# Performance work log

Measured on AMD Instinct MI355X. Metric: run time of the kernel, lower is better.

## Reference

```python
import jax, jax.numpy as jnp
import numpy as np

H = 1024
B_SZ = 4
L = 2048


def setup_inputs() -> dict:
    key = jax.random.key(0)
    ks = jax.random.split(key, 7)
    s_in = 1.0 / np.sqrt(H)
    x = jax.random.normal(ks[0], (B_SZ, L, H), dtype=jnp.float32)
    # torch nn.Linear weights: (out_features, in_features)
    W_proj = jax.random.uniform(ks[1], (4 * H, H), minval=-s_in, maxval=s_in, dtype=jnp.float32)
    W_delta = jax.random.uniform(ks[2], (H, H), minval=-s_in, maxval=s_in, dtype=jnp.float32)
    b_delta = jax.random.uniform(ks[3], (H,), minval=-s_in, maxval=s_in, dtype=jnp.float32)
    A = 0.02 * jax.random.normal(ks[4], (1, 1, H), dtype=jnp.float32)
    Bp = 0.02 * jax.random.normal(ks[5], (1, H, 1), dtype=jnp.float32)
    D = jnp.ones((1,), dtype=jnp.float32)
    return {"x": x, "W_proj": W_proj, "A": A, "Bp": Bp, "D": D, "W_delta": W_delta, "b_delta": b_delta}


def reference(x, W_proj, A, Bp, D, W_delta, b_delta):
    # x: (b, l, h)
    h = x.shape[-1]
    proj = x @ W_proj.T                                   # (b, l, 4h)
    delta, Bs, Cs, residual = jnp.split(proj, 4, axis=-1) # each (b, l, h)
    delta = jax.nn.softplus(delta @ W_delta.T + b_delta)  # (b, l, h)
    A1 = A[0, 0]       # (h,)
    B1 = Bp[0, :, 0]   # (h,)
    # discretization: dA[b,h,l] = exp(delta*A)[b,l,h] * B1[h] (n-dim of Bp has size 1)
    dA = jnp.exp(delta * A1) * B1                         # (b, l, h), layout transposed vs torch
    # dB[b,h,0,l] = cumsum_l(delta[b,l,h] * B1[h])
    dB = jnp.cumsum(delta * B1, axis=1)                   # (b, l, h)
    # selective_scan: y[b,h,l] = sum_n (dA[b,h,l]*u[b,h,n] + dB[b,h,0,l]) * C[b,h,n]
    # sum over n distributes: y = dA * sum_n(u*C) + dB * sum_n(C)
    uC = jnp.sum(x * Cs, axis=1, keepdims=True)           # (b, 1, h)
    Csum = jnp.sum(Cs, axis=1, keepdims=True)             # (b, 1, h)
    y = dA * uC + dB * Csum                               # (b, l, h)
    return y + residual * D
```

## Files before the change

### kernel.cpp

```cpp
#include <hip/hip_runtime.h>
#include <hip/hip_bf16.h>
#include <cstdint>

#define H 1024
#define BSZ 4
#define LSEQ 2048
#define M_TOT (BSZ*LSEQ)
#define NCH 32
#define LCH (LSEQ/NCH)

typedef __attribute__((ext_vector_type(4))) float  f32x4;
typedef __attribute__((ext_vector_type(2))) float  f32x2;
typedef __attribute__((ext_vector_type(8))) __bf16 bf16x8;
typedef __attribute__((ext_vector_type(4))) __bf16 bf16x4;
typedef __attribute__((ext_vector_type(2))) __bf16 bf16x2;

typedef __attribute__((address_space(1))) unsigned int as1_u32;
typedef __attribute__((address_space(3))) unsigned int as3_u32;

__device__ __forceinline__ void gld_lds16(const void* g, const void* l) {
    as1_u32* gp = reinterpret_cast<as1_u32*>((uintptr_t)g);
    as3_u32* lp = reinterpret_cast<as3_u32*>((uint32_t)(uintptr_t)l);
    __builtin_amdgcn_global_load_lds(gp, lp, 16, 0, 0);
}

template<int KT, int MODE>
__global__ __launch_bounds__(256, 3) void gemm_bt(
    const __bf16* __restrict__ A,
    const __bf16* __restrict__ B,
    __bf16* __restrict__ O0,
    __bf16* __restrict__ O2,
    const __bf16* __restrict__ xb,
    const float* __restrict__ bias,
    float* __restrict__ pD,
    float* __restrict__ pU,
    float* __restrict__ pC)
{
    constexpr int K = KT * 32;
    __shared__ __align__(16) __bf16 lds[17408];

    const int tid  = threadIdx.x;
    const int lane = tid & 63;
    const int wid  = tid >> 6;
    const int wr   = (wid >> 1) * 64;
    const int wc   = (wid & 1) * 64;
    const int l15  = lane & 15;
    const int quad = lane >> 4;

    const int row0 = blockIdx.y * 128;
    const int col0 = blockIdx.x * 128;

    const int srow = lane >> 2;
    const int soct = (lane & 3) ^ ((lane >> 3) & 3);
    const __bf16* ag0 = A + (size_t)(row0 + (wid    )*16 + srow) * K + soct*8;
    const __bf16* ag1 = A + (size_t)(row0 + (wid + 4)*16 + srow) * K + soct*8;
    const __bf16* bg0 = B + (size_t)(col0 + (wid    )*16 + srow) * K + soct*8;
    const __bf16* bg1 = B + (size_t)(col0 + (wid + 4)*16 + srow) * K + soct*8;
    const int lA0 = (wid    )*512;
    const int lA1 = (wid + 4)*512;
    const int lB0 = 4096 + (wid    )*512;
    const int lB1 = 4096 + (wid + 4)*512;

    const int sw = (l15 >> 1) & 3;
    int aoff[4], boff[4];
#pragma unroll
    for (int i = 0; i < 4; ++i) {
        aoff[i] =        ((wr + i*16 + l15) * 4 + (quad ^ sw)) * 8;
        boff[i] = 4096 + ((wc + i*16 + l15) * 4 + (quad ^ sw)) * 8;
    }

    f32x4 acc[4][4] = {};

    auto stage = [&](int buf) {
        __bf16* base = lds + buf * 8192;
        gld_lds16(ag0, base + lA0);
        gld_lds16(ag1, base + lA1);
        gld_lds16(bg0, base + lB0);
        gld_lds16(bg1, base + lB1);
        ag0 += 32; ag1 += 32; bg0 += 32; bg1 += 32;
    };
    auto compute = [&](int buf) {
        const __bf16* base = lds + buf * 8192;
        bf16x8 af[4], bf[4];
#pragma unroll
        for (int i = 0; i < 4; ++i) af[i] = *(const bf16x8*)(base + aoff[i]);
#pragma unroll
        for (int j = 0; j < 4; ++j) bf[j] = *(const bf16x8*)(base + boff[j]);
#pragma unroll
        for (int i = 0; i < 4; ++i)
#pragma unroll
            for (int j = 0; j < 4; ++j)
                acc[i][j] = __builtin_amdgcn_mfma_f32_16x16x32_bf16(
                    af[i], bf[j], acc[i][j], 0, 0, 0);
    };

    stage(0);
#pragma unroll 2
    for (int kt = 0; kt < KT; ++kt) {
        __syncthreads();
        if (kt + 1 < KT) stage((kt + 1) & 1);
        compute(kt & 1);
    }

    const int colb = (col0 & 1023) + wc + l15;
    const int rowb = row0 + wr + quad*4;

    if (MODE == 0) {
#pragma unroll
        for (int i = 0; i < 4; ++i)
#pragma unroll
            for (int j = 0; j < 4; ++j) {
                const int col = colb + j*16;
#pragma unroll
                for (int r = 0; r < 4; ++r)
                    O0[(size_t)(rowb + i*16 + r) * H + col] = (__bf16)acc[i][j][r];
            }
    } else {
        const int seg = col0 >> 10;
        if (seg == 0) {
            const int chunk = (row0 + wr) >> 6;
#pragma unroll
            for (int j = 0; j < 4; ++j) {
                const int col = colb + j*16;
                const float bv = bias[col];
                float s = 0.f;
#pragma unroll
                for (int i = 0; i < 4; ++i)
#pragma unroll
                    for (int r = 0; r < 4; ++r) {
                        float f = acc[i][j][r] + bv;
                        f = f > 15.f ? f : log1pf(expf(f));
                        O0[(size_t)(rowb + i*16 + r) * H + col] = (__bf16)f;
                        s += f;
                    }
                s += __shfl_down(s, 32); s += __shfl_down(s, 16);
                if (quad == 0) pD[chunk*H + col] = s;
            }
        } else if (seg == 1) {
            __syncthreads();
#pragma unroll
            for (int i = 0; i < 4; ++i)
#pragma unroll
                for (int j = 0; j < 4; ++j) {
                    const int lrow = wr + quad*4 + i*16;
                    const int lcol = wc + j*16 + l15;
#pragma unroll
                    for (int r = 0; r < 4; ++r)
                        lds[(lrow + r)*132 + lcol] = (__bf16)acc[i][j][r];
                }
            __syncthreads();
            float* pf = reinterpret_cast<float*>(lds + 16896);
            const int col  = tid & 127;
            const int half = tid >> 7;
            const int gcol = (col0 & 1023) + col;
            const int b    = row0 >> 11;
            float su = 0.f, sc = 0.f;
#pragma unroll 8
            for (int l = 0; l < 64; ++l) {
                const int row = half*64 + l;
                float cv = (float)lds[row*132 + col];
                float xv = (float)xb[(size_t)(row0 + row)*H + gcol];
                su += xv * cv;
                sc += cv;
            }
            if (half) { pf[col] = su; pf[128 + col] = sc; }
            __syncthreads();
            if (!half) {
                su += pf[col]; sc += pf[128 + col];
                atomicAdd(pU + b*H + gcol, su);
                atomicAdd(pC + b*H + gcol, sc);
            }
        } else {
#pragma unroll
            for (int i = 0; i < 4; ++i)
#pragma unroll
                for (int j = 0; j < 4; ++j) {
                    const int col = colb + j*16;
#pragma unroll
                    for (int r = 0; r < 4; ++r)
                        O2[(size_t)(rowb + i*16 + r) * H + col] = (__bf16)acc[i][j][r];
                }
        }
    }
}

#define XB 8192
#define PB 2048
#define DB 1024
#define TB 256
__global__ void cast_kernel(const float* __restrict__ x,
                            const float* __restrict__ Wp,
                            const float* __restrict__ Wd,
                            __bf16* __restrict__ xb,
                            __bf16* __restrict__ Wpb,
                            __bf16* __restrict__ Wdb,
                            __bf16* __restrict__ Wp1T)
{
    __shared__ __bf16 tlds[64*65];
    const int t = threadIdx.x;
    const int bidx = blockIdx.x;

    if (bidx < XB + PB + DB) {
        const f32x4* src; __bf16* dst; int si, di;
        if (bidx < XB) {
            int i = bidx*256 + t;
            src = (const f32x4*)x;  si = i; dst = xb;  di = i;
        } else if (bidx < XB + PB) {
            int j = (bidx - XB)*256 + t;
            int row = j >> 8, cf = j & 255;
            src = (const f32x4*)Wp; si = (2048 + row)*256 + cf;
            dst = Wpb; di = (1024 + row)*256 + cf;
        } else {
            int j = (bidx - XB - PB)*256 + t;
            src = (const f32x4*)Wd; si = j; dst = Wdb; di = j;
        }
        f32x4 v = src[si];
        bf16x4 o = { (__bf16)v[0], (__bf16)v[1], (__bf16)v[2], (__bf16)v[3] };
        *(bf16x4*)(dst + (size_t)di*4) = o;
    } else {
        int tt = bidx - (XB + PB + DB);
        int ty = tt >> 4, tx = tt & 15;
        int rb = t >> 4, cb = t & 15;
#pragma unroll
        for (int rr = 0; rr < 4; ++rr) {
            int row = rb*4 + rr;
            f32x4 v = *(const f32x4*)(Wp + (size_t)(ty*64 + row)*1024 + tx*64 + cb*4);
#pragma unroll
            for (int q = 0; q < 4; ++q)
                tlds[row*65 + cb*4 + q] = (__bf16)v[q];
        }
        __syncthreads();
#pragma unroll
        for (int rr = 0; rr < 4; ++rr) {
            int kk = rb*4 + rr;
            bf16x4 o = { tlds[(cb*4+0)*65 + kk], tlds[(cb*4+1)*65 + kk],
                         tlds[(cb*4+2)*65 + kk], tlds[(cb*4+3)*65 + kk] };
            *(bf16x4*)(Wp1T + (size_t)(tx*64 + kk)*1024 + ty*64 + cb*4) = o;
        }
    }
}

__global__ void scan_kernel(float* __restrict__ pD)
{
    int idx = blockIdx.x * 256 + threadIdx.x;
    int b = idx >> 10, h = idx & 1023;
    float run = 0.f;
    for (int c = 0; c < NCH; ++c) {
        int p = (b*NCH + c) * H + h;
        float t = pD[p]; pD[p] = run; run += t;
    }
}

__global__ void final_kernel(const __bf16* __restrict__ delta,
                             const __bf16* __restrict__ res,
                             const float* __restrict__ pD,
                             const float* __restrict__ uC,
                             const float* __restrict__ Csum,
                             const float* __restrict__ Av,
                             const float* __restrict__ Bv,
                             const float* __restrict__ Dv,
                             float* __restrict__ out)
{
    const int c = blockIdx.x, b = blockIdx.z;
    const int h0 = blockIdx.y * 512 + threadIdx.x * 2;
    const int pbase = (b*NCH + c)*H + h0;
    float run0 = pD[pbase], run1 = pD[pbase + 1];
    const f32x2 uc = *(const f32x2*)(uC + b*H + h0);
    const f32x2 cs = *(const f32x2*)(Csum + b*H + h0);
    const f32x2 a1 = *(const f32x2*)(Av + h0);
    const f32x2 b1 = *(const f32x2*)(Bv + h0);
    const float dd = Dv[0];
    size_t base = ((size_t)(b*LSEQ + c*LCH)) * H + h0;
    for (int l = 0; l < LCH; ++l) {
        size_t idx = base + (size_t)l * H;
        bf16x2 dv2 = *(const bf16x2*)(delta + idx);
        bf16x2 rs2 = *(const bf16x2*)(res + idx);
        float d0 = (float)dv2[0], d1v = (float)dv2[1];
        run0 += d0; run1 += d1v;
        f32x2 o;
        o[0] = expf(d0*a1[0])*b1[0]*uc[0] + run0*b1[0]*cs[0] + (float)rs2[0]*dd;
        o[1] = expf(d1v*a1[1])*b1[1]*uc[1] + run1*b1[1]*cs[1] + (float)rs2[1]*dd;
        *(f32x2*)(out + idx) = o;
    }
}

extern "C" void kernel_launch(void* const* d_in, const int* in_sizes, int n_in,
                              void* d_out, int out_size, void* d_ws, size_t ws_size,
                              hipStream_t stream)
{
    (void)in_sizes; (void)n_in; (void)out_size; (void)ws_size;
    const float* x  = (const float*)d_in[0];
    const float* Wp = (const float*)d_in[1];
    const float* Av = (const float*)d_in[2];
    const float* Bv = (const float*)d_in[3];
    const float* Dv = (const float*)d_in[4];
    const float* Wd = (const float*)d_in[5];
    const float* bd = (const float*)d_in[6];
    float* out = (float*)d_out;

    char* ws = (char*)d_ws;
    size_t o = 0;
    auto alloc = [&](size_t bytes) {
        void* p = ws + o; o += (bytes + 255) & ~(size_t)255; return p;
    };
    __bf16* xb   = (__bf16*)alloc((size_t)M_TOT * H * 2);
    __bf16* Wpb  = (__bf16*)alloc((size_t)3072 * H * 2);
    __bf16* Wdb  = (__bf16*)alloc((size_t)H * H * 2);
    __bf16* Wp1T = (__bf16*)alloc((size_t)H * H * 2);
    __bf16* resb = (__bf16*)alloc((size_t)M_TOT * H * 2);
    __bf16* db   = (__bf16*)alloc((size_t)M_TOT * H * 2);
    float*  pU   = (float*)alloc((size_t)BSZ * H * 4);
    float*  pC   = (float*)alloc((size_t)BSZ * H * 4);
    float*  pD   = (float*)alloc((size_t)BSZ * NCH * H * 4);

    hipMemsetAsync(pU, 0, (size_t)2 * BSZ * H * 4 + 256, stream);

    cast_kernel<<<XB + PB + DB + TB, 256, 0, stream>>>(
        x, Wp, Wd, xb, Wpb, Wdb, Wp1T);
    gemm_bt<32, 0><<<dim3(8, 8), 256, 0, stream>>>(
        Wdb, Wp1T, Wpb, nullptr, nullptr, nullptr, nullptr, nullptr, nullptr);
    gemm_bt<32, 2><<<dim3(24, 64), 256, 0, stream>>>(
        xb, Wpb, db, resb, xb, bd, pD, pU, pC);
    scan_kernel<<<16, 256, 0, stream>>>(pD);
    final_kernel<<<dim3(NCH, 2, BSZ), 256, 0, stream>>>(db, resb, pD, pU, pC,
                                                        Av, Bv, Dv, out);
}
```

Measured before the change: 238.5 us.

## Drop scan kernel and memset, use per-block partials and fast softplus

Removes the separate chunk-prefix scan kernel and the memset. The final kernel now sums the preceding chunk partials of delta and 16 per-row-block partials of uC and Csum itself. The Cs reduction epilogue replaces float atomics with vectorized 8-wide LDS and global loads, padded LDS rows and deterministic per-block partial stores. Softplus and the final exp use fast intrinsics. The cost is redundant prefix reads in the final kernel (up to 31 loads per thread) and slightly reduced accuracy from the fast math.

```diff
diff --git a/kernel.cpp b/kernel.cpp
--- a/kernel.cpp
+++ b/kernel.cpp
@@ -22,6 +22,10 @@
     as1_u32* gp = reinterpret_cast<as1_u32*>((uintptr_t)g);
     as3_u32* lp = reinterpret_cast<as3_u32*>((uint32_t)(uintptr_t)l);
     __builtin_amdgcn_global_load_lds(gp, lp, 16, 0, 0);
+}
+
+__device__ __forceinline__ float softplus_fast(float f) {
+    return fmaxf(f, 0.f) + __logf(1.f + __expf(-fabsf(f)));
 }
 
 template<int KT, int MODE>
@@ -33,8 +37,8 @@
     const __bf16* __restrict__ xb,
     const float* __restrict__ bias,
     float* __restrict__ pD,
-    float* __restrict__ pU,
-    float* __restrict__ pC)
+    float* __restrict__ pUp,
+    float* __restrict__ pCp)
 {
     constexpr int K = KT * 32;
     __shared__ __align__(16) __bf16 lds[17408];
@@ -128,8 +132,7 @@
                 for (int i = 0; i < 4; ++i)
 #pragma unroll
                     for (int r = 0; r < 4; ++r) {
-                        float f = acc[i][j][r] + bv;
-                        f = f > 15.f ? f : log1pf(expf(f));
+                        float f = softplus_fast(acc[i][j][r] + bv);
                         O0[(size_t)(rowb + i*16 + r) * H + col] = (__bf16)f;
                         s += f;
                     }
@@ -142,33 +145,48 @@
             for (int i = 0; i < 4; ++i)
 #pragma unroll
                 for (int j = 0; j < 4; ++j) {
-                    const int lrow = wr + quad*4 + i*16;
-                    const int lcol = wc + j*16 + l15;
+                    const int lrow0 = wr + quad*4 + i*16;
+                    const int lcol  = wc + j*16 + l15;
 #pragma unroll
                     for (int r = 0; r < 4; ++r)
-                        lds[(lrow + r)*132 + lcol] = (__bf16)acc[i][j][r];
+                        lds[(lrow0 + r)*136 + lcol] = (__bf16)acc[i][j][r];
                 }
             __syncthreads();
-            float* pf = reinterpret_cast<float*>(lds + 16896);
-            const int col  = tid & 127;
-            const int half = tid >> 7;
-            const int gcol = (col0 & 1023) + col;
-            const int b    = row0 >> 11;
-            float su = 0.f, sc = 0.f;
-#pragma unroll 8
-            for (int l = 0; l < 64; ++l) {
-                const int row = half*64 + l;
-                float cv = (float)lds[row*132 + col];
-                float xv = (float)xb[(size_t)(row0 + row)*H + gcol];
-                su += xv * cv;
-                sc += cv;
-            }
-            if (half) { pf[col] = su; pf[128 + col] = sc; }
+            const int g   = tid >> 4;
+            const int oct = tid & 15;
+            const int gc0 = (col0 & 1023) + oct*8;
+            float su[8] = {}, sc[8] = {};
+#pragma unroll
+            for (int rr = 0; rr < 8; ++rr) {
+                const int lrow = g*8 + rr;
+                bf16x8 cv = *(const bf16x8*)(lds + lrow*136 + oct*8);
+                bf16x8 xv = *(const bf16x8*)(xb + (size_t)(row0 + lrow)*H + gc0);
+#pragma unroll
+                for (int q = 0; q < 8; ++q) {
+                    float c = (float)cv[q];
+                    su[q] += (float)xv[q] * c;
+                    sc[q] += c;
+                }
+            }
+            float* pf = reinterpret_cast<float*>(lds);
             __syncthreads();
-            if (!half) {
-                su += pf[col]; sc += pf[128 + col];
-                atomicAdd(pU + b*H + gcol, su);
-                atomicAdd(pC + b*H + gcol, sc);
+#pragma unroll
+            for (int q = 0; q < 8; ++q) {
+                pf[g*128 + oct*8 + q]        = su[q];
+                pf[2048 + g*128 + oct*8 + q] = sc[q];
+            }
+            __syncthreads();
+            const int col = tid & 127;
+            const int rb  = row0 >> 7;
+            float s = 0.f;
+            if (tid < 128) {
+#pragma unroll
+                for (int g2 = 0; g2 < 16; ++g2) s += pf[g2*128 + col];
+                pUp[rb*H + (col0 & 1023) + col] = s;
+            } else {
+#pragma unroll
+                for (int g2 = 0; g2 < 16; ++g2) s += pf[2048 + g2*128 + col];
+                pCp[rb*H + (col0 & 1023) + col] = s;
             }
         } else {
 #pragma unroll
@@ -240,22 +258,11 @@
     }
 }
 
-__global__ void scan_kernel(float* __restrict__ pD)
-{
-    int idx = blockIdx.x * 256 + threadIdx.x;
-    int b = idx >> 10, h = idx & 1023;
-    float run = 0.f;
-    for (int c = 0; c < NCH; ++c) {
-        int p = (b*NCH + c) * H + h;
-        float t = pD[p]; pD[p] = run; run += t;
-    }
-}
-
 __global__ void final_kernel(const __bf16* __restrict__ delta,
                              const __bf16* __restrict__ res,
                              const float* __restrict__ pD,
-                             const float* __restrict__ uC,
-                             const float* __restrict__ Csum,
+                             const float* __restrict__ pUp,
+                             const float* __restrict__ pCp,
                              const float* __restrict__ Av,
                              const float* __restrict__ Bv,
                              const float* __restrict__ Dv,
@@ -263,10 +270,18 @@
 {
     const int c = blockIdx.x, b = blockIdx.z;
     const int h0 = blockIdx.y * 512 + threadIdx.x * 2;
-    const int pbase = (b*NCH + c)*H + h0;
-    float run0 = pD[pbase], run1 = pD[pbase + 1];
-    const f32x2 uc = *(const f32x2*)(uC + b*H + h0);
-    const f32x2 cs = *(const f32x2*)(Csum + b*H + h0);
+    float run0 = 0.f, run1 = 0.f;
+    for (int cp = 0; cp < c; ++cp) {
+        f32x2 v = *(const f32x2*)(pD + (b*NCH + cp)*H + h0);
+        run0 += v[0]; run1 += v[1];
+    }
+    float uc0 = 0.f, uc1 = 0.f, cs0 = 0.f, cs1 = 0.f;
+#pragma unroll
+    for (int i = 0; i < 16; ++i) {
+        f32x2 u = *(const f32x2*)(pUp + (b*16 + i)*H + h0);
+        f32x2 s = *(const f32x2*)(pCp + (b*16 + i)*H + h0);
+        uc0 += u[0]; uc1 += u[1]; cs0 += s[0]; cs1 += s[1];
+    }
     const f32x2 a1 = *(const f32x2*)(Av + h0);
     const f32x2 b1 = *(const f32x2*)(Bv + h0);
     const float dd = Dv[0];
@@ -278,8 +293,8 @@
         float d0 = (float)dv2[0], d1v = (float)dv2[1];
         run0 += d0; run1 += d1v;
         f32x2 o;
-        o[0] = expf(d0*a1[0])*b1[0]*uc[0] + run0*b1[0]*cs[0] + (float)rs2[0]*dd;
-        o[1] = expf(d1v*a1[1])*b1[1]*uc[1] + run1*b1[1]*cs[1] + (float)rs2[1]*dd;
+        o[0] = __expf(d0*a1[0])*b1[0]*uc0 + run0*b1[0]*cs0 + (float)rs2[0]*dd;
+        o[1] = __expf(d1v*a1[1])*b1[1]*uc1 + run1*b1[1]*cs1 + (float)rs2[1]*dd;
         *(f32x2*)(out + idx) = o;
     }
 }
@@ -309,19 +324,16 @@
     __bf16* Wp1T = (__bf16*)alloc((size_t)H * H * 2);
     __bf16* resb = (__bf16*)alloc((size_t)M_TOT * H * 2);
     __bf16* db   = (__bf16*)alloc((size_t)M_TOT * H * 2);
-    float*  pU   = (float*)alloc((size_t)BSZ * H * 4);
-    float*  pC   = (float*)alloc((size_t)BSZ * H * 4);
     float*  pD   = (float*)alloc((size_t)BSZ * NCH * H * 4);
-
-    hipMemsetAsync(pU, 0, (size_t)2 * BSZ * H * 4 + 256, stream);
+    float*  pUp  = (float*)alloc((size_t)64 * H * 4);
+    float*  pCp  = (float*)alloc((size_t)64 * H * 4);
 
     cast_kernel<<<XB + PB + DB + TB, 256, 0, stream>>>(
         x, Wp, Wd, xb, Wpb, Wdb, Wp1T);
     gemm_bt<32, 0><<<dim3(8, 8), 256, 0, stream>>>(
         Wdb, Wp1T, Wpb, nullptr, nullptr, nullptr, nullptr, nullptr, nullptr);
     gemm_bt<32, 2><<<dim3(24, 64), 256, 0, stream>>>(
-        xb, Wpb, db, resb, xb, bd, pD, pU, pC);
-    scan_kernel<<<16, 256, 0, stream>>>(pD);
-    final_kernel<<<dim3(NCH, 2, BSZ), 256, 0, stream>>>(db, resb, pD, pU, pC,
+        xb, Wpb, db, resb, xb, bd, pD, pUp, pCp);
+    final_kernel<<<dim3(NCH, 2, BSZ), 256, 0, stream>>>(db, resb, pD, pUp, pCp,
                                                         Av, Bv, Dv, out);
 }
```

Result: faster. 203.8 us (-14.6%).
